# Kernel tuning notes

Measured on AMD Instinct MI355X. Metric: run time of the kernel, lower is better.

Reference implementation:

```python
import math
import jax, jax.numpy as jnp
import numpy as np

N_HEADS = 16
TOPK_FACTOR = 0.5

def setup_inputs() -> dict:
    key = jax.random.key(0)
    ks = jax.random.split(key, 11)
    B, L, D = 2, 2048, 1024
    s = 0.02
    return {
        "q": jax.random.normal(ks[0], (B, L, D), jnp.float32),
        "k": jax.random.normal(ks[1], (B, L, D), jnp.float32),
        "v": jax.random.normal(ks[2], (B, L, D), jnp.float32),
        "Wq": jax.random.normal(ks[3], (D, D), jnp.float32) * s,
        "bq": jnp.zeros((D,), jnp.float32),
        "Wk": jax.random.normal(ks[4], (D, D), jnp.float32) * s,
        "bk": jnp.zeros((D,), jnp.float32),
        "Wv": jax.random.normal(ks[5], (D, D), jnp.float32) * s,
        "bv": jnp.zeros((D,), jnp.float32),
        "Wo": jax.random.normal(ks[6], (D, D), jnp.float32) * s,
        "bo": jnp.zeros((D,), jnp.float32),
    }

def reference(q, k, v, Wq, bq, Wk, bk, Wv, bv, Wo, bo):
    B, Lq, D = q.shape
    Lk = k.shape[1]
    H = N_HEADS
    d_k = D // H
    # projections -> [B, H, L, d_k]
    Q = (q @ Wq.T + bq).reshape(B, Lq, H, d_k).transpose(0, 2, 1, 3)
    K = (k @ Wk.T + bk).reshape(B, Lk, H, d_k).transpose(0, 2, 1, 3)
    V = (v @ Wv.T + bv).reshape(B, Lk, H, d_k).transpose(0, 2, 1, 3)
    # dense scores [B, H, Lq, Lk]
    scores = jnp.einsum("bhqd,bhkd->bhqk", Q, K) / math.sqrt(d_k)
    topk = max(1, int(TOPK_FACTOR * Lk))
    topk_scores, topk_idx = jax.lax.top_k(scores, topk)  # [B,H,Lq,topk]
    sm = jax.nn.softmax(topk_scores, axis=-1)
    # scatter softmax probs back into a zero [B,H,Lq,Lk] tensor (dropout in eval = identity)
    b_idx = jnp.arange(B)[:, None, None, None]
    h_idx = jnp.arange(H)[None, :, None, None]
    q_idx = jnp.arange(Lq)[None, None, :, None]
    attn = jnp.zeros_like(scores).at[b_idx, h_idx, q_idx, topk_idx].set(sm)
    ctx = jnp.einsum("bhqk,bhkd->bhqd", attn, V)
    ctx = ctx.transpose(0, 2, 1, 3).reshape(B, Lq, H * d_k)
    return ctx @ Wo.T + bo
```

## Files before the change

### kernel.cpp

```cpp
#include <hip/hip_runtime.h>
#include <math.h>

#define BATCH 2
#define SEQ 2048
#define DM 1024
#define NH 16
#define DH 64
#define TOPKN 1024
#define MROWS (BATCH * SEQ)

typedef float f32x4 __attribute__((ext_vector_type(4)));
typedef short s16x8 __attribute__((ext_vector_type(8)));
typedef short s16x4 __attribute__((ext_vector_type(4)));

#if __has_builtin(__builtin_amdgcn_mfma_f32_16x16x16_bf16)
#define MFMA1616(acc, a, b) acc = __builtin_amdgcn_mfma_f32_16x16x16_bf16(a, b, acc, 0, 0, 0)
#define MFMA1616_FENCE()
#elif __has_builtin(__builtin_amdgcn_mfma_f32_16x16x16bf16_1k)
#define MFMA1616(acc, a, b) acc = __builtin_amdgcn_mfma_f32_16x16x16bf16_1k(a, b, acc, 0, 0, 0)
#define MFMA1616_FENCE()
#else
#define MFMA1616(acc, a, b) \
  asm volatile("v_mfma_f32_16x16x16_bf16 %0, %1, %2, %0" : "+v"(acc) : "v"(a), "v"(b))
#define MFMA1616_FENCE() asm volatile("s_nop 7\ns_nop 7")
#endif

__device__ __forceinline__ unsigned short f2bf(float x) {
  unsigned u = __float_as_uint(x);
  return (unsigned short)((u + 0x7FFFu + ((u >> 16) & 1u)) >> 16);
}
__device__ __forceinline__ unsigned packHL(float x) {
  unsigned h = f2bf(x);
  float r = x - __uint_as_float(h << 16);
  unsigned l = f2bf(r);
  return h | (l << 16);
}

__global__ __launch_bounds__(256) void convW(const float* __restrict__ W,
                                             unsigned short* __restrict__ Whi,
                                             unsigned short* __restrict__ Wlo) {
  int i = (blockIdx.x * 256 + threadIdx.x) * 4;
  float4 x = *(const float4*)&W[i];
  float xs[4] = {x.x, x.y, x.z, x.w};
  union { s16x4 v; unsigned short s[4]; } hu, lu;
#pragma unroll
  for (int e = 0; e < 4; ++e) {
    unsigned short hb = f2bf(xs[e]);
    hu.s[e] = hb;
    lu.s[e] = f2bf(xs[e] - __uint_as_float((unsigned)hb << 16));
  }
  *(s16x4*)&Whi[i] = hu.v;
  *(s16x4*)&Wlo[i] = lu.v;
}

template <int ASRC, int MODE>
__global__ __launch_bounds__(256) void gemm_mfma(
    const void* __restrict__ Asrc, const unsigned short* __restrict__ Whi,
    const unsigned short* __restrict__ Wlo, const float* __restrict__ bias,
    void* __restrict__ out0, void* __restrict__ out1) {
  __shared__ unsigned short Ah[128][64], Al[128][64];
  __shared__ unsigned short Bh[64][64], Bl[64][64];

  const int f = blockIdx.x;
  const int xcd = f & 7, s = f >> 3;
  const int bm = xcd * 4 + (s >> 4);
  const int bn = s & 15;
  const int m0g = bm * 128, n0g = bn * 64;
  const int t = threadIdx.x, w = t >> 6, lane = t & 63;
  const int g = lane >> 4, c = lane & 15;
  const int wm = w >> 1, wn = w & 1;

  f32x4 acc[4][2];
#pragma unroll
  for (int i = 0; i < 4; ++i)
#pragma unroll
    for (int j = 0; j < 2; ++j) acc[i][j] = (f32x4){0.f, 0.f, 0.f, 0.f};

#pragma unroll 1
  for (int k0 = 0; k0 < 1024; k0 += 64) {
#pragma unroll
    for (int i = 0; i < 4; ++i) {
      int oid = t * 4 + i;
      int r = oid >> 3, j = oid & 7;
      union { s16x8 v; unsigned short sh[8]; } hu, lu;
      if (ASRC == 0) {
        const float* src = (const float*)Asrc + (size_t)(m0g + r) * 1024 + k0 + j * 8;
        float4 x0 = *(const float4*)src, x1 = *(const float4*)(src + 4);
        float xs[8] = {x0.x, x0.y, x0.z, x0.w, x1.x, x1.y, x1.z, x1.w};
#pragma unroll
        for (int e = 0; e < 8; ++e) {
          unsigned u = __float_as_uint(xs[e]);
          hu.sh[e] = (unsigned short)(u >> 16);
          lu.sh[e] = f2bf(xs[e] - __uint_as_float(u & 0xFFFF0000u));
        }
      } else {
        const unsigned* src = (const unsigned*)Asrc + (size_t)(m0g + r) * 1024 + k0 + j * 8;
        uint4 u0 = *(const uint4*)src, u1 = *(const uint4*)(src + 4);
        unsigned us[8] = {u0.x, u0.y, u0.z, u0.w, u1.x, u1.y, u1.z, u1.w};
#pragma unroll
        for (int e = 0; e < 8; ++e) {
          hu.sh[e] = (unsigned short)(us[e] & 0xFFFFu);
          lu.sh[e] = (unsigned short)(us[e] >> 16);
        }
      }
      int od = (j ^ (r & 7)) * 8;
      *(s16x8*)&Ah[r][od] = hu.v;
      *(s16x8*)&Al[r][od] = lu.v;
    }
#pragma unroll
    for (int i = 0; i < 4; ++i) {
      int oid = t * 4 + i;
      int pl = oid >> 9, idx = oid & 511, r = idx >> 3, j = idx & 7;
      const unsigned short* src = (pl ? Wlo : Whi) + (size_t)(n0g + r) * 1024 + k0 + j * 8;
      uint4 d = *(const uint4*)src;
      int od = (j ^ (r & 7)) * 8;
      if (pl) *(uint4*)&Bl[r][od] = d; else *(uint4*)&Bh[r][od] = d;
    }
    __syncthreads();
#pragma unroll
    for (int k2 = 0; k2 < 2; ++k2) {
      s16x8 ah[4], al4[4], bh[2], bl[2];
      int ob = ((k2 * 4 + g) ^ (c & 7)) * 8;
#pragma unroll
      for (int i = 0; i < 4; ++i) {
        int r = wm * 64 + i * 16 + c;
        ah[i] = *(const s16x8*)&Ah[r][ob];
        al4[i] = *(const s16x8*)&Al[r][ob];
      }
#pragma unroll
      for (int j = 0; j < 2; ++j) {
        int r = wn * 32 + j * 16 + c;
        bh[j] = *(const s16x8*)&Bh[r][ob];
        bl[j] = *(const s16x8*)&Bl[r][ob];
      }
#pragma unroll
      for (int i = 0; i < 4; ++i)
#pragma unroll
        for (int j = 0; j < 2; ++j) {
          acc[i][j] = __builtin_amdgcn_mfma_f32_16x16x32_bf16(ah[i], bh[j], acc[i][j], 0, 0, 0);
          acc[i][j] = __builtin_amdgcn_mfma_f32_16x16x32_bf16(ah[i], bl[j], acc[i][j], 0, 0, 0);
          acc[i][j] = __builtin_amdgcn_mfma_f32_16x16x32_bf16(al4[i], bh[j], acc[i][j], 0, 0, 0);
        }
    }
    __syncthreads();
  }

#pragma unroll
  for (int j = 0; j < 2; ++j) {
    const int col = n0g + wn * 32 + j * 16 + c;
    const float bj = bias[col];
#pragma unroll
    for (int i = 0; i < 4; ++i) {
      const int row0 = m0g + wm * 64 + i * 16 + g * 4;
      if (MODE == 0) {
        float* O = (float*)out0;
#pragma unroll
        for (int rr = 0; rr < 4; ++rr)
          O[(size_t)(row0 + rr) * 1024 + col] = acc[i][j][rr] + bj;
      } else if (MODE == 1) {
        unsigned* Q = (unsigned*)out0;
#pragma unroll
        for (int rr = 0; rr < 4; ++rr)
          Q[(size_t)(row0 + rr) * 1024 + col] = packHL((acc[i][j][rr] + bj) * 0.125f);
      } else if (MODE == 2) {
        unsigned short* Khi = (unsigned short*)out0;
        unsigned short* Klo = (unsigned short*)out1;
#pragma unroll
        for (int rr = 0; rr < 4; ++rr) {
          float x = acc[i][j][rr] + bj;
          unsigned short hb = f2bf(x);
          Khi[(size_t)(row0 + rr) * 1024 + col] = hb;
          Klo[(size_t)(row0 + rr) * 1024 + col] = f2bf(x - __uint_as_float((unsigned)hb << 16));
        }
      } else {
        unsigned short* Vt = (unsigned short*)out0;
        int b = row0 >> 11, l0 = row0 & (SEQ - 1);
        int h = col >> 6, dh = col & 63;
        union { s16x4 v; unsigned short sh[4]; } vv;
#pragma unroll
        for (int rr = 0; rr < 4; ++rr) vv.sh[rr] = f2bf(acc[i][j][rr] + bj);
        *(s16x4*)&Vt[(((size_t)b * NH + h) * DH + dh) * SEQ + l0] = vv.v;
      }
    }
  }
}

__global__ __launch_bounds__(512, 4) void attn_mfma(
    const unsigned* __restrict__ QHL, const unsigned short* __restrict__ Khi,
    const unsigned short* __restrict__ Klo, const unsigned short* __restrict__ Vt,
    unsigned* __restrict__ CtxP) {
  __shared__ __align__(16) unsigned scnt[2][16][8];
  __shared__ __align__(16) float szum[16][8];
  __shared__ __align__(16) float ctxp[8][16][72];

  int wg = blockIdx.x;
  wg = (wg & 7) * 512 + (wg >> 3);
  const int bh = wg >> 7, qt = wg & 127;
  const int b = bh >> 4, h = bh & 15;
  const int q0 = qt * 16;
  const int t = threadIdx.x, w = t >> 6, lane = t & 63;
  const int g = lane >> 4, c = lane & 15;
  const size_t rowb = (size_t)b * SEQ;

  s16x8 qhi[2], qlo[2];
  {
    const unsigned* qp = QHL + (rowb + q0 + c) * DM + h * DH + g * 8;
#pragma unroll
    for (int ds = 0; ds < 2; ++ds) {
      unsigned uw[8];
      *(uint4*)&uw[0] = *(const uint4*)(qp + ds * 32);
      *(uint4*)&uw[4] = *(const uint4*)(qp + ds * 32 + 4);
      union { s16x8 v; unsigned u[4]; } hi_, lo_;
#pragma unroll
      for (int p = 0; p < 4; ++p) {
        hi_.u[p] = (uw[2 * p] & 0xFFFFu) | (uw[2 * p + 1] << 16);
        lo_.u[p] = (uw[2 * p] >> 16) | (uw[2 * p + 1] & 0xFFFF0000u);
      }
      qhi[ds] = hi_.v; qlo[ds] = lo_.v;
    }
  }

  unsigned pk[16][2];
  {
    const f32x4 ZZ = (f32x4){0.f, 0.f, 0.f, 0.f};
    const size_t kcol = (size_t)h * DH + g * 8;
#pragma unroll
    for (int tt = 0; tt < 16; ++tt) {
      const size_t krow = (rowb + w * 256 + tt * 16 + c) * DM + kcol;
      s16x8 kh0 = *(const s16x8*)(Khi + krow);
      s16x8 kh1 = *(const s16x8*)(Khi + krow + 32);
      s16x8 kl0 = *(const s16x8*)(Klo + krow);
      s16x8 kl1 = *(const s16x8*)(Klo + krow + 32);
      f32x4 a = __builtin_amdgcn_mfma_f32_16x16x32_bf16(kh0, qhi[0], ZZ, 0, 0, 0);
      a = __builtin_amdgcn_mfma_f32_16x16x32_bf16(kh1, qhi[1], a, 0, 0, 0);
      a = __builtin_amdgcn_mfma_f32_16x16x32_bf16(kl0, qhi[0], a, 0, 0, 0);
      a = __builtin_amdgcn_mfma_f32_16x16x32_bf16(kl1, qhi[1], a, 0, 0, 0);
      a = __builtin_amdgcn_mfma_f32_16x16x32_bf16(kh0, qlo[0], a, 0, 0, 0);
      a = __builtin_amdgcn_mfma_f32_16x16x32_bf16(kh1, qlo[1], a, 0, 0, 0);
      unsigned u0 = (unsigned)fminf(fmaf(a[0], 8192.f, 32768.5f), 65535.f);
      unsigned u1 = (unsigned)fminf(fmaf(a[1], 8192.f, 32768.5f), 65535.f);
      unsigned u2 = (unsigned)fminf(fmaf(a[2], 8192.f, 32768.5f), 65535.f);
      unsigned u3 = (unsigned)fminf(fmaf(a[3], 8192.f, 32768.5f), 65535.f);
      pk[tt][0] = u0 | (u1 << 16);
      pk[tt][1] = u2 | (u3 << 16);
    }
  }

  unsigned lo = 30720u, hi = 34816u;
#pragma unroll 1
  for (int it = 0; it < 12; ++it) {
    const int par = it & 1;
    const unsigned mid = (lo + hi) >> 1;
    int cnt = 0;
#pragma unroll
    for (int tt = 0; tt < 16; ++tt)
#pragma unroll
      for (int j = 0; j < 2; ++j) {
        unsigned p = pk[tt][j];
        cnt += ((p & 0xFFFFu) >= mid) ? 1 : 0;
        cnt += ((p >> 16) >= mid) ? 1 : 0;
      }
    cnt += __shfl_xor(cnt, 16);
    cnt += __shfl_xor(cnt, 32);
    if (lane < 16) scnt[par][c][w] = (unsigned)cnt;
    __syncthreads();
    uint4 c0 = *(uint4*)&scnt[par][c][0];
    uint4 c1 = *(uint4*)&scnt[par][c][4];
    int tot = (int)(c0.x + c0.y + c0.z + c0.w + c1.x + c1.y + c1.z + c1.w);
    bool ge = tot >= TOPKN;
    lo = ge ? mid : lo;
    hi = ge ? hi : mid;
  }
  const unsigned T = lo;

  const float C1 = 1.44269504f / 8192.0f;
  const float C2 = -49152.0f * (1.44269504f / 8192.0f);
  f32x4 opv[4];
#pragma unroll
  for (int j = 0; j < 4; ++j) opv[j] = (f32x4){0.f, 0.f, 0.f, 0.f};
  float z = 0.f;
  {
    const unsigned short* vb0 = Vt + ((size_t)bh * DH + c) * SEQ + w * 256 + g * 4;
#pragma unroll
    for (int kt = 0; kt < 16; ++kt) {
      unsigned p0 = pk[kt][0], p1 = pk[kt][1];
      unsigned u0 = p0 & 0xFFFFu, u1 = p0 >> 16;
      unsigned u2 = p1 & 0xFFFFu, u3 = p1 >> 16;
      float e0 = (u0 >= T) ? exp2f(fmaf((float)u0, C1, C2)) : 0.f;
      float e1 = (u1 >= T) ? exp2f(fmaf((float)u1, C1, C2)) : 0.f;
      float e2 = (u2 >= T) ? exp2f(fmaf((float)u2, C1, C2)) : 0.f;
      float e3 = (u3 >= T) ? exp2f(fmaf((float)u3, C1, C2)) : 0.f;
      z += (e0 + e1) + (e2 + e3);
      union { s16x4 v; unsigned u[2]; } pb;
      pb.u[0] = ((__float_as_uint(e0) + 0x8000u) >> 16) |
                ((__float_as_uint(e1) + 0x8000u) & 0xFFFF0000u);
      pb.u[1] = ((__float_as_uint(e2) + 0x8000u) >> 16) |
                ((__float_as_uint(e3) + 0x8000u) & 0xFFFF0000u);
#pragma unroll
      for (int j = 0; j < 4; ++j) {
        s16x4 va = *(const s16x4*)(vb0 + (size_t)j * 16 * SEQ + kt * 16);
        MFMA1616(opv[j], va, pb.v);
      }
    }
    MFMA1616_FENCE();
  }

  z += __shfl_xor(z, 16);
  z += __shfl_xor(z, 32);
  if (lane < 16) szum[c][w] = z;
#pragma unroll
  for (int j = 0; j < 4; ++j)
    *(f32x4*)&ctxp[w][c][j * 16 + g * 4] = opv[j];
  __syncthreads();
  if (w < 4) {
    float4 z0 = *(float4*)&szum[c][0];
    float4 z1 = *(float4*)&szum[c][4];
    float rinv = 1.f / (z0.x + z0.y + z0.z + z0.w + z1.x + z1.y + z1.z + z1.w);
    f32x4 ssum = (f32x4){0.f, 0.f, 0.f, 0.f};
#pragma unroll
    for (int w2 = 0; w2 < 8; ++w2)
      ssum += *(const f32x4*)&ctxp[w2][c][w * 16 + g * 4];
    unsigned ov[4];
    ov[0] = packHL(ssum[0] * rinv);
    ov[1] = packHL(ssum[1] * rinv);
    ov[2] = packHL(ssum[2] * rinv);
    ov[3] = packHL(ssum[3] * rinv);
    *(uint4*)&CtxP[(rowb + q0 + c) * DM + h * DH + w * 16 + g * 4] = *(uint4*)&ov[0];
  }
}

extern "C" void kernel_launch(void* const* d_in, const int* in_sizes, int n_in,
                              void* d_out, int out_size, void* d_ws, size_t ws_size,
                              hipStream_t stream) {
  const float* q  = (const float*)d_in[0];
  const float* k  = (const float*)d_in[1];
  const float* v  = (const float*)d_in[2];
  const float* Wq = (const float*)d_in[3];
  const float* bq = (const float*)d_in[4];
  const float* Wk = (const float*)d_in[5];
  const float* bk = (const float*)d_in[6];
  const float* Wv = (const float*)d_in[7];
  const float* bv = (const float*)d_in[8];
  const float* Wo = (const float*)d_in[9];
  const float* bo = (const float*)d_in[10];
  float* out = (float*)d_out;

  char* ws = (char*)d_ws;
  unsigned* QHL       = (unsigned*)ws;
  unsigned short* Khi = (unsigned short*)(ws + (16u << 20));
  unsigned short* Klo = (unsigned short*)(ws + (24u << 20));
  unsigned short* Vt  = (unsigned short*)(ws + (32u << 20));
  unsigned short* Whi = (unsigned short*)(ws + (40u << 20));
  unsigned short* Wlo = (unsigned short*)(ws + (42u << 20));

  convW<<<1024, 256, 0, stream>>>(Wq, Whi, Wlo);
  gemm_mfma<0, 1><<<512, 256, 0, stream>>>(q, Whi, Wlo, bq, QHL, nullptr);
  convW<<<1024, 256, 0, stream>>>(Wk, Whi, Wlo);
  gemm_mfma<0, 2><<<512, 256, 0, stream>>>(k, Whi, Wlo, bk, Khi, Klo);
  convW<<<1024, 256, 0, stream>>>(Wv, Whi, Wlo);
  gemm_mfma<0, 3><<<512, 256, 0, stream>>>(v, Whi, Wlo, bv, Vt, nullptr);
  attn_mfma<<<BATCH * NH * (SEQ / 16), 512, 0, stream>>>(QHL, Khi, Klo, Vt, QHL);
  convW<<<1024, 256, 0, stream>>>(Wo, Whi, Wlo);
  gemm_mfma<1, 0><<<512, 256, 0, stream>>>(QHL, Whi, Wlo, bo, out, nullptr);
}
```

Measured before the change: 713.6 us.

## Transpose quantized scores through LDS so each half-wave bisects one row barrier-free

Before this change, the 12-step bisection for the top-k threshold did one block-wide __syncthreads and an LDS count exchange per step, because every wave held a slice of every query row. Now each wave writes its packed 16-bit scores into a 16x1028 shared buffer. After a single barrier, each half-wave loads one full query row into registers and runs all 12 bisection steps using only wave shuffles, then publishes the threshold through LDS. This removes 11 block barriers. In exchange it adds a transpose through about 66KB of LDS (aliased with the context buffer), which may lower occupancy relative to launch_bounds(512,4).

```diff
diff --git a/kernel.cpp b/kernel.cpp
--- a/kernel.cpp
+++ b/kernel.cpp
@@ -189,9 +189,11 @@
     const unsigned* __restrict__ QHL, const unsigned short* __restrict__ Khi,
     const unsigned short* __restrict__ Klo, const unsigned short* __restrict__ Vt,
     unsigned* __restrict__ CtxP) {
-  __shared__ __align__(16) unsigned scnt[2][16][8];
-  __shared__ __align__(16) float szum[16][8];
-  __shared__ __align__(16) float ctxp[8][16][72];
+  __shared__ __align__(16) char smem[16 * 1028 * 4];
+  __shared__ __align__(16) unsigned Tlds[16];
+  unsigned (*sc)[1028] = (unsigned(*)[1028])smem;
+  float (*ctxp)[16][72] = (float(*)[16][72])smem;
+  float (*szum)[8] = (float(*)[8])(smem + 8 * 16 * 72 * 4);
 
   int wg = blockIdx.x;
   wg = (wg & 7) * 512 + (wg >> 3);
@@ -246,32 +248,52 @@
     }
   }
 
-  unsigned lo = 30720u, hi = 34816u;
+#pragma unroll
+  for (int tt = 0; tt < 16; ++tt) {
+    int col = w * 128 + tt * 8 + g * 2;
+    sc[c][col] = pk[tt][0];
+    sc[c][col + 1] = pk[tt][1];
+  }
+  __syncthreads();
+
+  {
+    const int r = 2 * w + (lane >> 5);
+    const int hl = lane & 31;
+    uint4 ts[8];
+#pragma unroll
+    for (int i = 0; i < 8; ++i)
+      ts[i] = *(const uint4*)&sc[r][hl * 4 + i * 128];
+
+    unsigned lo = 30720u, hi = 34816u;
 #pragma unroll 1
-  for (int it = 0; it < 12; ++it) {
-    const int par = it & 1;
-    const unsigned mid = (lo + hi) >> 1;
-    int cnt = 0;
-#pragma unroll
-    for (int tt = 0; tt < 16; ++tt)
-#pragma unroll
-      for (int j = 0; j < 2; ++j) {
-        unsigned p = pk[tt][j];
-        cnt += ((p & 0xFFFFu) >= mid) ? 1 : 0;
-        cnt += ((p >> 16) >= mid) ? 1 : 0;
-      }
-    cnt += __shfl_xor(cnt, 16);
-    cnt += __shfl_xor(cnt, 32);
-    if (lane < 16) scnt[par][c][w] = (unsigned)cnt;
-    __syncthreads();
-    uint4 c0 = *(uint4*)&scnt[par][c][0];
-    uint4 c1 = *(uint4*)&scnt[par][c][4];
-    int tot = (int)(c0.x + c0.y + c0.z + c0.w + c1.x + c1.y + c1.z + c1.w);
-    bool ge = tot >= TOPKN;
-    lo = ge ? mid : lo;
-    hi = ge ? hi : mid;
-  }
-  const unsigned T = lo;
+    for (int it = 0; it < 12; ++it) {
+      const unsigned mid = (lo + hi) >> 1;
+      int cnt = 0;
+#pragma unroll
+      for (int i = 0; i < 8; ++i) {
+        unsigned a0 = ts[i].x, a1 = ts[i].y, a2 = ts[i].z, a3 = ts[i].w;
+        cnt += ((a0 & 0xFFFFu) >= mid) ? 1 : 0;
+        cnt += ((a0 >> 16) >= mid) ? 1 : 0;
+        cnt += ((a1 & 0xFFFFu) >= mid) ? 1 : 0;
+        cnt += ((a1 >> 16) >= mid) ? 1 : 0;
+        cnt += ((a2 & 0xFFFFu) >= mid) ? 1 : 0;
+        cnt += ((a2 >> 16) >= mid) ? 1 : 0;
+        cnt += ((a3 & 0xFFFFu) >= mid) ? 1 : 0;
+        cnt += ((a3 >> 16) >= mid) ? 1 : 0;
+      }
+      cnt += __shfl_xor(cnt, 1);
+      cnt += __shfl_xor(cnt, 2);
+      cnt += __shfl_xor(cnt, 4);
+      cnt += __shfl_xor(cnt, 8);
+      cnt += __shfl_xor(cnt, 16);
+      bool ge = cnt >= TOPKN;
+      lo = ge ? mid : lo;
+      hi = ge ? hi : mid;
+    }
+    if ((lane & 31) == 0) Tlds[r] = lo;
+  }
+  __syncthreads();
+  const unsigned T = Tlds[c];
 
   const float C1 = 1.44269504f / 8192.0f;
   const float C2 = -49152.0f * (1.44269504f / 8192.0f);
```

Result: no change. 710.2 us (-0.5%).
